# Kernel optimization log

Measured on AMD Instinct MI355X. Metric: run time of the kernel, lower is better.

Reference implementation:

```python
import jax, jax.numpy as jnp
import numpy as np

MARGIN = 0.3
BIG = 1e6  # matches the 1000000.0 additive mask in the torch code


def setup_inputs() -> dict:
    key = jax.random.key(0)
    k1, k2 = jax.random.split(key)
    embeddings = jax.random.normal(k1, (4096, 512), dtype=jnp.float32)
    labels = jax.random.randint(k2, (4096,), 0, 512)
    return {"embeddings": embeddings, "labels": labels}


def reference(embeddings, labels):
    # Pairwise euclidean distances (torch.cdist p=2) via the GEMM identity,
    # clamped before sqrt for numerical safety on the zero diagonal.
    sq = jnp.sum(embeddings * embeddings, axis=1)                      # [N]
    d2 = sq[:, None] + sq[None, :] - 2.0 * (embeddings @ embeddings.T)  # [N, N]
    dist = jnp.sqrt(jnp.maximum(d2, 1e-12))

    pos_mask = labels[None, :] == labels[:, None]   # [N, N] bool
    neg_mask = ~pos_mask

    # Hardest positive per anchor (self-distance 0 is harmless under max).
    hp = jnp.max(dist * pos_mask.astype(dist.dtype), axis=1)           # [N]

    # Semi-hard negatives: hp < d(a, n) < hp + margin, different label.
    semi_hard = (dist > hp[:, None]) & (dist < hp[:, None] + MARGIN) & neg_mask
    has_semi_hard = jnp.sum(semi_hard) > 0

    # Fallback: hardest (farthest) negative; semi-hard branch: closest semi-hard.
    hn_fallback = jnp.max(dist * neg_mask.astype(dist.dtype), axis=1)
    hn_semi = jnp.min(dist + (1.0 - semi_hard.astype(dist.dtype)) * BIG, axis=1)
    hn = jnp.where(has_semi_hard, hn_semi, hn_fallback)                # [N]

    triplet = jax.nn.relu(hp - hn + MARGIN)                            # [N]
    num_valid = jnp.sum((triplet > 0).astype(triplet.dtype))
    loss = jnp.where(num_valid > 0,
                     jnp.sum(triplet) / jnp.maximum(num_valid, 1.0),
                     jnp.mean(triplet))
    return loss
```

## Files before the change

kernel.cpp:

```cpp
#include <hip/hip_runtime.h>
#include <math.h>


constexpr float MARGIN = 0.3f;

typedef _Float16 half8    __attribute__((ext_vector_type(8)));
typedef float    floatx16 __attribute__((ext_vector_type(16)));

#define GLD_LDS16(gp, lp)                                                              \
    __builtin_amdgcn_global_load_lds(                                                  \
        (const __attribute__((address_space(1))) void*)(gp),                           \
        (__attribute__((address_space(3))) void*)(lp), 16, 0, 0)

__global__ __launch_bounds__(256)
void prep_kernel(const float* __restrict__ e, _Float16* __restrict__ pan,
                 float* __restrict__ sq, unsigned int* __restrict__ hp,
                 unsigned int* __restrict__ hn_fall, unsigned int* __restrict__ hn_semi,
                 unsigned int* __restrict__ bars, int N, int D) {
    if (blockIdx.x == 0 && threadIdx.x < 32) bars[threadIdx.x * 32] = 0u;
    const int r0  = blockIdx.x * 32;
    const int p   = r0 >> 7;
    const int rl  = r0 & 127;
    const int r   = threadIdx.x >> 3;
    const int c8  = threadIdx.x & 7;
    const int row = r0 + r;
    const float* er = e + (size_t)row * D;
    float s = 0.f;
    #pragma unroll
    for (int it = 0; it < 8; ++it) {
        const int kw = c8 + it * 8;
        const float4 x0 = *(const float4*)&er[kw * 8];
        const float4 x1 = *(const float4*)&er[kw * 8 + 4];
        const float xv[8] = {x0.x, x0.y, x0.z, x0.w, x1.x, x1.y, x1.z, x1.w};
        half8 hi, lo;
        #pragma unroll
        for (int j = 0; j < 8; ++j) {
            _Float16 h = (_Float16)xv[j];
            hi[j] = h;
            lo[j] = (_Float16)(xv[j] - (float)h);
            s += xv[j] * xv[j];
        }
        *(half8*)&pan[((size_t)(p * 128 + kw) * 128 + rl + r) * 8]      = hi;
        *(half8*)&pan[((size_t)(p * 128 + 64 + kw) * 128 + rl + r) * 8] = lo;
    }
    s += __shfl_down(s, 4, 8);
    s += __shfl_down(s, 2, 8);
    s += __shfl_down(s, 1, 8);
    if (c8 == 0) {
        sq[row]      = s;
        hp[row]      = 0u;
        hn_fall[row] = 0u;
        hn_semi[row] = 0x7f800000u;
    }
}

__global__ __launch_bounds__(512, 4)
void fused_kernel(const _Float16* __restrict__ pan, const int* __restrict__ labels,
                  const float* __restrict__ sq,
                  unsigned int* __restrict__ hp,
                  unsigned int* __restrict__ hn_fall,
                  unsigned int* __restrict__ hn_semi,
                  unsigned int* __restrict__ bars,
                  float* __restrict__ out,
                  int N, int D, unsigned int nrowblocks, unsigned int nblocks) {
    __shared__ __attribute__((aligned(16))) _Float16 S[2][12288];
    __shared__ float sq_r[256], sq_c[128], hp_r[256];
    __shared__ int   lab_r[256], lab_c[128];
    __shared__ int   lastflag;

    const int tid  = threadIdx.x;
    const int lane = tid & 63;
    const int wave = tid >> 6;
    const int wr = (wave >> 1) * 64;
    const int wc = (wave & 1) * 64;
    const int mrow = lane & 31;
    const int half_id = lane >> 5;

    const int j  = blockIdx.x & 7;
    const int i  = blockIdx.x >> 3;
    const int px = (j & 3) * 8 + (i & 7);
    const int py = (j >> 2) * 8 + (i >> 3);
    const int rowBase = py * 256;
    const int colBase = px * 128;

    if (tid < 256) {
        sq_r[tid]  = sq[rowBase + tid];
        lab_r[tid] = labels[rowBase + tid];
    } else if (tid < 384) {
        const int t = tid - 256;
        sq_c[t]  = sq[colBase + t];
        lab_c[t] = labels[colBase + t];
    }

    floatx16 acc[2][2];
    #pragma unroll
    for (int a = 0; a < 2; ++a)
        #pragma unroll
        for (int b = 0; b < 2; ++b)
            #pragma unroll
            for (int r = 0; r < 16; ++r) acc[a][b][r] = 0.f;

    auto stage = [&](int b, int kkv) {
        #pragma unroll
        for (int t = 0; t < 3; ++t) {
            const int s = wave * 3 + t;
            int kcl, p, row0, lofs;
            if (s < 16) {
                const int rq = s & 3;
                kcl  = s >> 2;
                p    = 2 * py + (rq >> 1);
                row0 = (rq & 1) * 64;
                lofs = (kcl * 256 + rq * 64) * 8;
            } else {
                const int u = s - 16;
                kcl  = u >> 1;
                p    = px;
                row0 = (u & 1) * 64;
                lofs = 8192 + (kcl * 128 + row0) * 8;
            }
            const int kc = (kcl < 2) ? (2 * kkv + kcl) : (64 + 2 * kkv + (kcl - 2));
            const _Float16* g = pan + ((size_t)(p * 128 + kc) * 128 + row0 + lane) * 8;
            GLD_LDS16(g, &S[b][lofs]);
        }
    };

    stage(0, 0);

    #pragma unroll 1
    for (int kk = 0; kk < 32; ++kk) {
        const int b = kk & 1;
        __syncthreads();
        if (kk + 1 < 32) stage(b ^ 1, kk + 1);
        const int rA = wr + mrow, cB = wc + mrow;
        const half8 ah0 = *(const half8*)&S[b][(half_id * 256 + rA) * 8];
        const half8 ah1 = *(const half8*)&S[b][(half_id * 256 + rA + 32) * 8];
        const half8 al0 = *(const half8*)&S[b][((2 + half_id) * 256 + rA) * 8];
        const half8 al1 = *(const half8*)&S[b][((2 + half_id) * 256 + rA + 32) * 8];
        const half8 bh0 = *(const half8*)&S[b][8192 + (half_id * 128 + cB) * 8];
        const half8 bh1 = *(const half8*)&S[b][8192 + (half_id * 128 + cB + 32) * 8];
        const half8 bl0 = *(const half8*)&S[b][8192 + ((2 + half_id) * 128 + cB) * 8];
        const half8 bl1 = *(const half8*)&S[b][8192 + ((2 + half_id) * 128 + cB + 32) * 8];
        acc[0][0] = __builtin_amdgcn_mfma_f32_32x32x16_f16(bh0, ah0, acc[0][0], 0, 0, 0);
        acc[0][1] = __builtin_amdgcn_mfma_f32_32x32x16_f16(bh0, ah1, acc[0][1], 0, 0, 0);
        acc[1][0] = __builtin_amdgcn_mfma_f32_32x32x16_f16(bh1, ah0, acc[1][0], 0, 0, 0);
        acc[1][1] = __builtin_amdgcn_mfma_f32_32x32x16_f16(bh1, ah1, acc[1][1], 0, 0, 0);
        acc[0][0] = __builtin_amdgcn_mfma_f32_32x32x16_f16(bl0, ah0, acc[0][0], 0, 0, 0);
        acc[0][1] = __builtin_amdgcn_mfma_f32_32x32x16_f16(bl0, ah1, acc[0][1], 0, 0, 0);
        acc[1][0] = __builtin_amdgcn_mfma_f32_32x32x16_f16(bl1, ah0, acc[1][0], 0, 0, 0);
        acc[1][1] = __builtin_amdgcn_mfma_f32_32x32x16_f16(bl1, ah1, acc[1][1], 0, 0, 0);
        acc[0][0] = __builtin_amdgcn_mfma_f32_32x32x16_f16(bh0, al0, acc[0][0], 0, 0, 0);
        acc[0][1] = __builtin_amdgcn_mfma_f32_32x32x16_f16(bh0, al1, acc[0][1], 0, 0, 0);
        acc[1][0] = __builtin_amdgcn_mfma_f32_32x32x16_f16(bh1, al0, acc[1][0], 0, 0, 0);
        acc[1][1] = __builtin_amdgcn_mfma_f32_32x32x16_f16(bh1, al1, acc[1][1], 0, 0, 0);
    }

    float sqr[2]; int labr[2];
    #pragma unroll
    for (int ai = 0; ai < 2; ++ai) {
        sqr[ai]  = sq_r[wr + ai * 32 + mrow];
        labr[ai] = lab_r[wr + ai * 32 + mrow];
    }

    #pragma unroll
    for (int ai = 0; ai < 2; ++ai) {
        float vp = 0.f, vn = 0.f;
        #pragma unroll
        for (int bj = 0; bj < 2; ++bj) {
            #pragma unroll
            for (int r = 0; r < 16; ++r) {
                const int c = wc + bj * 32 + (r & 3) + 8 * (r >> 2) + 4 * half_id;
                float d = sqrtf(fmaxf(sqr[ai] + sq_c[c] - 2.0f * acc[bj][ai][r], 1e-12f));
                const bool pos = (labr[ai] == lab_c[c]);
                vp = fmaxf(vp, pos ? d : 0.f);
                vn = fmaxf(vn, pos ? 0.f : d);
            }
        }
        vp = fmaxf(vp, __shfl_xor(vp, 32, 64));
        vn = fmaxf(vn, __shfl_xor(vn, 32, 64));
        if (half_id == 0) {
            atomicMax(&hp[rowBase + wr + ai * 32 + mrow],      __float_as_uint(vp));
            atomicMax(&hn_fall[rowBase + wr + ai * 32 + mrow], __float_as_uint(vn));
        }
    }

    __syncthreads();
    unsigned int* ctr = &bars[py * 32];
    if (tid == 0) {
        __threadfence();
        atomicAdd(ctr, 1u);
        while (__hip_atomic_load(ctr, __ATOMIC_ACQUIRE, __HIP_MEMORY_SCOPE_AGENT)
               < nrowblocks)
            __builtin_amdgcn_s_sleep(32);
    }
    __syncthreads();
    if (tid < 256)
        hp_r[tid] = __uint_as_float(__hip_atomic_load(&hp[rowBase + tid],
                                    __ATOMIC_RELAXED, __HIP_MEMORY_SCOPE_AGENT));
    __syncthreads();

    #pragma unroll
    for (int ai = 0; ai < 2; ++ai) {
        const float hpv = hp_r[wr + ai * 32 + mrow];
        float vm = __builtin_inff();
        #pragma unroll
        for (int bj = 0; bj < 2; ++bj) {
            #pragma unroll
            for (int r = 0; r < 16; ++r) {
                const int c = wc + bj * 32 + (r & 3) + 8 * (r >> 2) + 4 * half_id;
                float d = sqrtf(fmaxf(sqr[ai] + sq_c[c] - 2.0f * acc[bj][ai][r], 1e-12f));
                const bool cand = (labr[ai] != lab_c[c]) && (d > hpv);
                vm = fminf(vm, cand ? d : __builtin_inff());
            }
        }
        vm = fminf(vm, __shfl_xor(vm, 32, 64));
        if (half_id == 0)
            atomicMin(&hn_semi[rowBase + wr + ai * 32 + mrow], __float_as_uint(vm));
    }

    __syncthreads();
    if (tid == 0) {
        __threadfence();
        unsigned int old = atomicAdd(&bars[992], 1u);
        lastflag = (old == nblocks - 1) ? 1 : 0;
    }
    __syncthreads();
    if (!lastflag) return;
    if (tid == 0) __threadfence();
    __syncthreads();

    float* FS = (float*)&S[0][0];
    int*   IC = (int*)(FS + 512);
    int*   IA = IC + 512;
    int any = 0;
    for (int r = tid; r < N; r += 512) {
        float h  = __uint_as_float(__hip_atomic_load(&hp[r],      __ATOMIC_RELAXED, __HIP_MEMORY_SCOPE_AGENT));
        float hs = __uint_as_float(__hip_atomic_load(&hn_semi[r], __ATOMIC_RELAXED, __HIP_MEMORY_SCOPE_AGENT));
        any |= (hs < h + MARGIN) ? 1 : 0;
    }
    IA[tid] = any;
    __syncthreads();
    for (int s = 256; s; s >>= 1) {
        if (tid < s) IA[tid] |= IA[tid + s];
        __syncthreads();
    }
    const bool has_semi = IA[0] != 0;
    float sum = 0.f; int valid = 0;
    for (int r = tid; r < N; r += 512) {
        float h  = __uint_as_float(__hip_atomic_load(&hp[r], __ATOMIC_RELAXED, __HIP_MEMORY_SCOPE_AGENT));
        float hn = has_semi
            ? __uint_as_float(__hip_atomic_load(&hn_semi[r], __ATOMIC_RELAXED, __HIP_MEMORY_SCOPE_AGENT))
            : __uint_as_float(__hip_atomic_load(&hn_fall[r], __ATOMIC_RELAXED, __HIP_MEMORY_SCOPE_AGENT));
        float t = fmaxf(h - hn + MARGIN, 0.f);
        if (!(t > 0.f)) t = 0.f;
        sum += t;
        valid += (t > 0.f) ? 1 : 0;
    }
    FS[tid] = sum; IC[tid] = valid;
    __syncthreads();
    for (int s = 256; s; s >>= 1) {
        if (tid < s) { FS[tid] += FS[tid + s]; IC[tid] += IC[tid + s]; }
        __syncthreads();
    }
    if (tid == 0) {
        float total = FS[0]; int v = IC[0];
        out[0] = (v > 0) ? (total / (float)v) : (total / (float)N);
    }
}

extern "C" void kernel_launch(void* const* d_in, const int* in_sizes, int n_in,
                              void* d_out, int out_size, void* d_ws, size_t ws_size,
                              hipStream_t stream) {
    const float* e      = (const float*)d_in[0];
    const int*   labels = (const int*)d_in[1];
    const int N = in_sizes[1];
    const int D = in_sizes[0] / N;
    float* out = (float*)d_out;

    float*        sq      = (float*)d_ws;
    unsigned int* hp      = (unsigned int*)d_ws + N;
    unsigned int* hn_fall = hp + N;
    unsigned int* hn_semi = hn_fall + N;
    unsigned int* bars    = hn_semi + N;

    const size_t small_bytes = ((size_t)(4 * N + 1024) * 4 + 255) & ~(size_t)255;
    _Float16* pan = (_Float16*)((char*)d_ws + small_bytes);

    prep_kernel<<<N / 32, 256, 0, stream>>>(e, pan, sq, hp, hn_fall, hn_semi, bars, N, D);

    const int ntx = N / 128, nty = N / 256;
    fused_kernel<<<ntx * nty, 512, 0, stream>>>(pan, labels, sq, hp, hn_fall, hn_semi,
                                                bars, out, N, D,
                                                (unsigned)ntx, (unsigned)(ntx * nty));
}
```

Baseline: 142.3 us.

## Triple-buffer GEMM LDS staging with vmcnt waits and remap prep kernel

The fused kernel's LDS staging moves from double to triple buffering. Loads are issued two K-steps ahead, and explicit s_waitcnt vmcnt plus raw s_barrier replace __syncthreads, so global-to-LDS loads overlap more MFMA work. MFMA sections get raised wave priority with s_setprio. The prep kernel now handles 8 rows per block with a shared-memory reduction, launching four times as many blocks for better memory parallelism. This costs extra LDS per block, which may reduce occupancy, and the hand-written wait counts add a risk of correctness errors.

```diff
diff --git a/kernel.cpp b/kernel.cpp
--- a/kernel.cpp
+++ b/kernel.cpp
@@ -17,18 +17,19 @@
                  float* __restrict__ sq, unsigned int* __restrict__ hp,
                  unsigned int* __restrict__ hn_fall, unsigned int* __restrict__ hn_semi,
                  unsigned int* __restrict__ bars, int N, int D) {
+    __shared__ float red[256];
     if (blockIdx.x == 0 && threadIdx.x < 32) bars[threadIdx.x * 32] = 0u;
-    const int r0  = blockIdx.x * 32;
+    const int r0  = blockIdx.x * 8;
     const int p   = r0 >> 7;
     const int rl  = r0 & 127;
-    const int r   = threadIdx.x >> 3;
-    const int c8  = threadIdx.x & 7;
+    const int r   = threadIdx.x & 7;
+    const int c8  = threadIdx.x >> 3;
     const int row = r0 + r;
     const float* er = e + (size_t)row * D;
     float s = 0.f;
     #pragma unroll
-    for (int it = 0; it < 8; ++it) {
-        const int kw = c8 + it * 8;
+    for (int it = 0; it < 2; ++it) {
+        const int kw = c8 + it * 32;
         const float4 x0 = *(const float4*)&er[kw * 8];
         const float4 x1 = *(const float4*)&er[kw * 8 + 4];
         const float xv[8] = {x0.x, x0.y, x0.z, x0.w, x1.x, x1.y, x1.z, x1.w};
@@ -43,14 +44,17 @@
         *(half8*)&pan[((size_t)(p * 128 + kw) * 128 + rl + r) * 8]      = hi;
         *(half8*)&pan[((size_t)(p * 128 + 64 + kw) * 128 + rl + r) * 8] = lo;
     }
-    s += __shfl_down(s, 4, 8);
-    s += __shfl_down(s, 2, 8);
-    s += __shfl_down(s, 1, 8);
-    if (c8 == 0) {
-        sq[row]      = s;
-        hp[row]      = 0u;
-        hn_fall[row] = 0u;
-        hn_semi[row] = 0x7f800000u;
+    red[threadIdx.x] = s;
+    __syncthreads();
+    if (threadIdx.x < 8) {
+        float t = 0.f;
+        #pragma unroll
+        for (int c = 0; c < 32; ++c) t += red[threadIdx.x + 8 * c];
+        const int rw = r0 + threadIdx.x;
+        sq[rw]      = t;
+        hp[rw]      = 0u;
+        hn_fall[rw] = 0u;
+        hn_semi[rw] = 0x7f800000u;
     }
 }
 
@@ -63,7 +67,7 @@
                   unsigned int* __restrict__ bars,
                   float* __restrict__ out,
                   int N, int D, unsigned int nrowblocks, unsigned int nblocks) {
-    __shared__ __attribute__((aligned(16))) _Float16 S[2][12288];
+    __shared__ __attribute__((aligned(16))) _Float16 S[3][12288];
     __shared__ float sq_r[256], sq_c[128], hp_r[256];
     __shared__ int   lab_r[256], lab_c[128];
     __shared__ int   lastflag;
@@ -100,7 +104,7 @@
             #pragma unroll
             for (int r = 0; r < 16; ++r) acc[a][b][r] = 0.f;
 
-    auto stage = [&](int b, int kkv) {
+    auto stage = [&](int bufid, int kkv) {
         #pragma unroll
         for (int t = 0; t < 3; ++t) {
             const int s = wave * 3 + t;
@@ -120,26 +124,32 @@
             }
             const int kc = (kcl < 2) ? (2 * kkv + kcl) : (64 + 2 * kkv + (kcl - 2));
             const _Float16* g = pan + ((size_t)(p * 128 + kc) * 128 + row0 + lane) * 8;
-            GLD_LDS16(g, &S[b][lofs]);
+            GLD_LDS16(g, &S[bufid][lofs]);
         }
     };
 
     stage(0, 0);
-
+    stage(1, 1);
+    asm volatile("s_waitcnt vmcnt(3)" ::: "memory");
+    __builtin_amdgcn_s_barrier();
+    asm volatile("" ::: "memory");
+
+    int b = 0;
     #pragma unroll 1
     for (int kk = 0; kk < 32; ++kk) {
-        const int b = kk & 1;
-        __syncthreads();
-        if (kk + 1 < 32) stage(b ^ 1, kk + 1);
         const int rA = wr + mrow, cB = wc + mrow;
-        const half8 ah0 = *(const half8*)&S[b][(half_id * 256 + rA) * 8];
-        const half8 ah1 = *(const half8*)&S[b][(half_id * 256 + rA + 32) * 8];
-        const half8 al0 = *(const half8*)&S[b][((2 + half_id) * 256 + rA) * 8];
-        const half8 al1 = *(const half8*)&S[b][((2 + half_id) * 256 + rA + 32) * 8];
-        const half8 bh0 = *(const half8*)&S[b][8192 + (half_id * 128 + cB) * 8];
-        const half8 bh1 = *(const half8*)&S[b][8192 + (half_id * 128 + cB + 32) * 8];
-        const half8 bl0 = *(const half8*)&S[b][8192 + ((2 + half_id) * 128 + cB) * 8];
-        const half8 bl1 = *(const half8*)&S[b][8192 + ((2 + half_id) * 128 + cB + 32) * 8];
+        const _Float16* Sb = &S[b][0];
+        const half8 ah0 = *(const half8*)&Sb[(half_id * 256 + rA) * 8];
+        const half8 ah1 = *(const half8*)&Sb[(half_id * 256 + rA + 32) * 8];
+        const half8 al0 = *(const half8*)&Sb[((2 + half_id) * 256 + rA) * 8];
+        const half8 al1 = *(const half8*)&Sb[((2 + half_id) * 256 + rA + 32) * 8];
+        const half8 bh0 = *(const half8*)&Sb[8192 + (half_id * 128 + cB) * 8];
+        const half8 bh1 = *(const half8*)&Sb[8192 + (half_id * 128 + cB + 32) * 8];
+        const half8 bl0 = *(const half8*)&Sb[8192 + ((2 + half_id) * 128 + cB) * 8];
+        const half8 bl1 = *(const half8*)&Sb[8192 + ((2 + half_id) * 128 + cB + 32) * 8];
+        int sb = b + 2; if (sb >= 3) sb -= 3;
+        if (kk + 2 < 32) stage(sb, kk + 2);
+        __builtin_amdgcn_s_setprio(1);
         acc[0][0] = __builtin_amdgcn_mfma_f32_32x32x16_f16(bh0, ah0, acc[0][0], 0, 0, 0);
         acc[0][1] = __builtin_amdgcn_mfma_f32_32x32x16_f16(bh0, ah1, acc[0][1], 0, 0, 0);
         acc[1][0] = __builtin_amdgcn_mfma_f32_32x32x16_f16(bh1, ah0, acc[1][0], 0, 0, 0);
@@ -152,6 +162,12 @@
         acc[0][1] = __builtin_amdgcn_mfma_f32_32x32x16_f16(bh0, al1, acc[0][1], 0, 0, 0);
         acc[1][0] = __builtin_amdgcn_mfma_f32_32x32x16_f16(bh1, al0, acc[1][0], 0, 0, 0);
         acc[1][1] = __builtin_amdgcn_mfma_f32_32x32x16_f16(bh1, al1, acc[1][1], 0, 0, 0);
+        __builtin_amdgcn_s_setprio(0);
+        if (kk < 30) { asm volatile("s_waitcnt vmcnt(3)" ::: "memory"); }
+        else         { asm volatile("s_waitcnt vmcnt(0)" ::: "memory"); }
+        __builtin_amdgcn_s_barrier();
+        asm volatile("" ::: "memory");
+        b = (b == 2) ? 0 : b + 1;
     }
 
     float sqr[2]; int labr[2];
@@ -285,7 +301,7 @@
     const size_t small_bytes = ((size_t)(4 * N + 1024) * 4 + 255) & ~(size_t)255;
     _Float16* pan = (_Float16*)((char*)d_ws + small_bytes);
 
-    prep_kernel<<<N / 32, 256, 0, stream>>>(e, pan, sq, hp, hn_fall, hn_semi, bars, N, D);
+    prep_kernel<<<N / 8, 256, 0, stream>>>(e, pan, sq, hp, hn_fall, hn_semi, bars, N, D);
 
     const int ntx = N / 128, nty = N / 256;
     fused_kernel<<<ntx * nty, 512, 0, stream>>>(pan, labels, sq, hp, hn_fall, hn_semi,
```

Result: slower. 149.3 us (+4.9%).
